# Optimization experiments

Measured on AMD Instinct MI355X. Metric: run time of the kernel, lower is better.

## Reference

```python
import jax, jax.numpy as jnp
import numpy as np

N_NODES = 100000
N_EDGES = 1000000
D = 64            # in_channels == heads*hidden_channels
OUT = 64          # out_channels
L = 3             # local_layers
RVQ = 3           # residual VQ levels per layer
CODES = 16
BN_EPS = 1e-5
COMMIT_W = 0.25


def _l2n(v, eps=1e-12):
    return v / (jnp.linalg.norm(v, axis=-1, keepdims=True) + eps)


def setup_inputs() -> dict:
    key = jax.random.key(0)
    ks = jax.random.split(key, 16)
    s = 1.0 / np.sqrt(D)
    inp = {
        "x": jax.random.normal(ks[0], (N_NODES, D), jnp.float32),
        "edge_index": jax.random.randint(ks[1], (2, N_EDGES), 0, N_NODES, jnp.int64),
        # SAGEConv: lin_l (applied to mean-aggregated neighbors, with bias), lin_r (root, no bias)
        "Wa": jax.random.uniform(ks[2], (L, D, D), jnp.float32, -s, s),
        "ba": jax.random.uniform(ks[3], (L, D), jnp.float32, -s, s),
        "Wr": jax.random.uniform(ks[4], (L, D, D), jnp.float32, -s, s),
        # skip Linear per layer
        "Wl": jax.random.uniform(ks[5], (L, D, D), jnp.float32, -s, s),
        "bl": jax.random.uniform(ks[6], (L, D), jnp.float32, -s, s),
        # BatchNorm affine
        "gamma": jnp.ones((L, D), jnp.float32),
        "beta": jnp.zeros((L, D), jnp.float32),
        # residual-VQ codebooks: [layer, rvq_level, codes, dim]
        "codebooks": jax.random.normal(ks[7], (L, RVQ, CODES, D), jnp.float32),
        # heads
        "Wp": jax.random.uniform(ks[8], (D, OUT), jnp.float32, -s, s),
        "bp": jax.random.uniform(ks[9], (OUT,), jnp.float32, -s, s),
        "Wg": jax.random.uniform(ks[10], (D, L * RVQ), jnp.float32, -s, s),
        "bg": jax.random.uniform(ks[11], (L * RVQ,), jnp.float32, -s, s),
    }
    return inp


def _sage_conv(x, src, dst, Wa, ba, Wr):
    # mean aggregation of source features onto destinations
    summed = jax.ops.segment_sum(x[src], dst, num_segments=N_NODES)
    cnt = jax.ops.segment_sum(jnp.ones((src.shape[0],), x.dtype), dst, num_segments=N_NODES)
    mean = summed / jnp.maximum(cnt, 1.0)[:, None]
    out = mean @ Wa + ba + x @ Wr
    return _l2n(out)  # normalize=True


def _residual_vq(x, cbs):
    # cosine-sim residual VQ, 3 levels; returns (quantized_sum, ids [N,RVQ], commit_loss)
    residual = x
    quant = jnp.zeros_like(x)
    loss = jnp.zeros((), x.dtype)
    ids = []
    for r in range(RVQ):
        cb = _l2n(cbs[r])                       # [CODES, D]
        sim = _l2n(residual) @ cb.T             # [N, CODES]
        idx = jnp.argmax(sim, axis=-1)          # [N]
        q = cb[idx]                             # [N, D]
        loss = loss + COMMIT_W * jnp.mean((jax.lax.stop_gradient(q) - residual) ** 2)
        q_st = residual + jax.lax.stop_gradient(q - residual)  # straight-through
        quant = quant + q_st
        residual = residual - jax.lax.stop_gradient(q)
        ids.append(idx)
    return quant, jnp.stack(ids, axis=1), loss


def reference(x, edge_index, Wa, ba, Wr, Wl, bl, gamma, beta, codebooks, Wp, bp, Wg, bg):
    src, dst = edge_index[0], edge_index[1]
    h = x  # in_dropout: identity at inference
    x_local = jnp.zeros((N_NODES, D), x.dtype)
    total_commit = jnp.zeros((), x.dtype)
    id_list = []
    for i in range(L):
        h = _sage_conv(h, src, dst, Wa[i], ba[i], Wr[i]) + (h @ Wl[i] + bl[i])
        # BatchNorm1d (batch statistics)
        mu = jnp.mean(h, axis=0)
        var = jnp.var(h, axis=0)
        h = (h - mu) * jax.lax.rsqrt(var + BN_EPS) * gamma[i] + beta[i]
        h = jax.nn.relu(h)  # dropout: identity at inference
        x_local = x_local + h
        _, ids, closs = _residual_vq(h, codebooks[i])
        total_commit = total_commit + closs
        id_list.append(ids)
    id_concat = jnp.concatenate(id_list, axis=1)  # [N, L*RVQ]
    gnn_id = x_local @ Wg + bg
    pred = x_local @ Wp + bp
    return (pred, total_commit, id_concat, gnn_id)
```

## Files before the change

kernel.cpp:

```cpp
#include <hip/hip_runtime.h>
#include <math.h>

#define NN 100000
#define NE 1000000
#define D 64
#define L 3
#define RVQ 3
#define CODES 16
#define BN_EPS 1e-5f
#define COMMIT_W 0.25f

#define GRID_A 2048

#define OFS_ROWPTR 0
#define OFS_CNT    100016
#define OFS_CURSOR 200032
#define OFS_BSUMS  300048
#define OFS_BOFFS  300176
#define OFS_STATS  300304
#define OFS_CSR    300800
#define OFS_HA     1300800
#define OFS_HB     7700800
#define OFS_XLOC   14100800
#define OFS_PART   20500800

#define OUT_PRED   0
#define OUT_COMMIT (NN * D)
#define OUT_IDS    (NN * D + 1)
#define OUT_GNN    (NN * D + 1 + NN * (L * RVQ))

static __device__ __forceinline__ float waveSum(float v) {
    #pragma unroll
    for (int off = 32; off; off >>= 1) v += __shfl_xor(v, off, 64);
    return v;
}

__global__ void k_count(const int* __restrict__ dst, int* __restrict__ cnt) {
    int e = blockIdx.x * blockDim.x + threadIdx.x;
    if (e < NE) atomicAdd(&cnt[dst[e]], 1);
}

#define SCAN_B 1024
__global__ void k_scan1(const int* __restrict__ cnt, int* __restrict__ rowptr,
                        int* __restrict__ bsums) {
    __shared__ int sm[SCAN_B];
    int t = threadIdx.x;
    int i = blockIdx.x * SCAN_B + t;
    int v = (i < NN) ? cnt[i] : 0;
    sm[t] = v;
    __syncthreads();
    for (int off = 1; off < SCAN_B; off <<= 1) {
        int add = (t >= off) ? sm[t - off] : 0;
        __syncthreads();
        sm[t] += add;
        __syncthreads();
    }
    if (i < NN) rowptr[i + 1] = sm[t];
    if (t == SCAN_B - 1) bsums[blockIdx.x] = sm[t];
}

__global__ void k_scan2(const int* __restrict__ bsums, int* __restrict__ boffs, int nb) {
    __shared__ int sm[SCAN_B];
    int t = threadIdx.x;
    int orig = (t < nb) ? bsums[t] : 0;
    sm[t] = orig;
    __syncthreads();
    for (int off = 1; off < SCAN_B; off <<= 1) {
        int add = (t >= off) ? sm[t - off] : 0;
        __syncthreads();
        sm[t] += add;
        __syncthreads();
    }
    if (t < nb) boffs[t] = sm[t] - orig;
}

__global__ void k_scan3(int* __restrict__ rowptr, const int* __restrict__ boffs) {
    int i = blockIdx.x * SCAN_B + threadIdx.x;
    if (i < NN) rowptr[i + 1] += boffs[blockIdx.x];
    if (i == 0) rowptr[0] = 0;
}

__global__ void k_cursor(const int* __restrict__ rowptr, int* __restrict__ cursor) {
    int i = blockIdx.x * blockDim.x + threadIdx.x;
    if (i < NN) cursor[i] = rowptr[i];
}

__global__ void k_fill(const int* __restrict__ src, const int* __restrict__ dst,
                       int* __restrict__ cursor, int* __restrict__ csr_src) {
    int e = blockIdx.x * blockDim.x + threadIdx.x;
    if (e < NE) {
        int p = atomicAdd(&cursor[dst[e]], 1);
        csr_src[p] = src[e];
    }
}

__global__ void k_sortrows(const int* __restrict__ rowptr, int* __restrict__ csr) {
    int n = blockIdx.x * blockDim.x + threadIdx.x;
    if (n >= NN) return;
    int r0 = rowptr[n], r1 = rowptr[n + 1];
    for (int i = r0 + 1; i < r1; ++i) {
        int v = csr[i];
        int j = i - 1;
        while (j >= r0 && csr[j] > v) { csr[j + 1] = csr[j]; --j; }
        csr[j + 1] = v;
    }
}

__global__ __launch_bounds__(256) void k_gather(
    const float* __restrict__ h, const int* __restrict__ rowptr,
    const int* __restrict__ csr_src, float* __restrict__ mean_out) {
    int t = threadIdx.x;
    int lane = t & 63, wid = t >> 6;
    int n = blockIdx.x * 4 + wid;
    if (n >= NN) return;

    int r0 = rowptr[n], r1 = rowptr[n + 1];
    float s = 0.f;
    for (int base = r0; base < r1; base += 64) {
        int last = r1 - 1;
        int ii = base + lane;
        int idx = csr_src[(ii <= last) ? ii : last];
        int m = r1 - base;
        if (m > 64) m = 64;
        int j = 0;
        for (; j + 8 <= m; j += 8) {
            int i0 = __shfl(idx, j + 0, 64), i1 = __shfl(idx, j + 1, 64);
            int i2 = __shfl(idx, j + 2, 64), i3 = __shfl(idx, j + 3, 64);
            int i4 = __shfl(idx, j + 4, 64), i5 = __shfl(idx, j + 5, 64);
            int i6 = __shfl(idx, j + 6, 64), i7 = __shfl(idx, j + 7, 64);
            float v0 = h[i0 * D + lane], v1 = h[i1 * D + lane];
            float v2 = h[i2 * D + lane], v3 = h[i3 * D + lane];
            float v4 = h[i4 * D + lane], v5 = h[i5 * D + lane];
            float v6 = h[i6 * D + lane], v7 = h[i7 * D + lane];
            s += v0; s += v1; s += v2; s += v3;
            s += v4; s += v5; s += v6; s += v7;
        }
        for (; j + 4 <= m; j += 4) {
            int i0 = __shfl(idx, j + 0, 64), i1 = __shfl(idx, j + 1, 64);
            int i2 = __shfl(idx, j + 2, 64), i3 = __shfl(idx, j + 3, 64);
            float v0 = h[i0 * D + lane], v1 = h[i1 * D + lane];
            float v2 = h[i2 * D + lane], v3 = h[i3 * D + lane];
            s += v0; s += v1; s += v2; s += v3;
        }
        for (; j < m; ++j) {
            int i0 = __shfl(idx, j, 64);
            s += h[i0 * D + lane];
        }
    }
    float deg = (float)(r1 - r0);
    mean_out[n * D + lane] = s / fmaxf(deg, 1.0f);
}

__global__ __launch_bounds__(256) void k_matvec(
    const float* __restrict__ h, float* __restrict__ hp,
    const float* __restrict__ Wa, const float* __restrict__ ba,
    const float* __restrict__ Wr, const float* __restrict__ Wl,
    const float* __restrict__ bl, float* __restrict__ partials) {
    __shared__ float red[2][4][D];
    __shared__ float lbuf[4][2][128];
    int t = threadIdx.x, lane = t & 63, wid = t >> 6;

    float wa[D], wr[D], wl[D];
    #pragma unroll
    for (int k = 0; k < D; ++k) {
        wa[k] = Wa[k * D + lane];
        wr[k] = Wr[k * D + lane];
        wl[k] = Wl[k * D + lane];
    }
    float bav = ba[lane], blv = bl[lane];

    int wg = blockIdx.x * 4 + wid;
    const int wstep = GRID_A * 4;
    float accS = 0.f, accQ = 0.f;

    int seg = lane >> 4;
    int sl  = lane & 15;

    {
        float4 v = {0.f, 0.f, 0.f, 0.f};
        if (seg == 0)      v = *(const float4*)(hp + (size_t)wg * D + 4 * sl);
        else if (seg == 1) v = *(const float4*)(h  + (size_t)wg * D + 4 * sl);
        if (seg < 2) *(float4*)&lbuf[wid][0][seg * 64 + 4 * sl] = v;
    }

    int p = 0;
    for (int n = wg; n < NN; n += wstep) {
        int nn = n + wstep;
        bool havepf = (nn < NN);
        float4 pf = {0.f, 0.f, 0.f, 0.f};
        if (havepf && seg < 2) {
            const float* srcp = (seg == 0) ? hp : h;
            pf = *(const float4*)(srcp + (size_t)nn * D + 4 * sl);
        }

        const float* mb = &lbuf[wid][p][0];
        const float* hb = &lbuf[wid][p][64];
        float a = 0.f, r = 0.f, lv = 0.f;
        #pragma unroll
        for (int j = 0; j < 16; ++j) {
            float4 m4 = *(const float4*)(mb + 4 * j);
            float4 h4 = *(const float4*)(hb + 4 * j);
            a += m4.x * wa[4 * j + 0]; r += h4.x * wr[4 * j + 0]; lv += h4.x * wl[4 * j + 0];
            a += m4.y * wa[4 * j + 1]; r += h4.y * wr[4 * j + 1]; lv += h4.y * wl[4 * j + 1];
            a += m4.z * wa[4 * j + 2]; r += h4.z * wr[4 * j + 2]; lv += h4.z * wl[4 * j + 2];
            a += m4.w * wa[4 * j + 3]; r += h4.w * wr[4 * j + 3]; lv += h4.w * wl[4 * j + 3];
        }
        float sage = a + bav + r;
        float ss = waveSum(sage * sage);
        float inv = 1.0f / (sqrtf(ss) + 1e-12f);
        float hpv = sage * inv + lv + blv;
        hp[(size_t)n * D + lane] = hpv;
        accS += hpv;
        accQ += hpv * hpv;

        if (havepf && seg < 2)
            *(float4*)&lbuf[wid][p ^ 1][seg * 64 + 4 * sl] = pf;
        p ^= 1;
    }

    red[0][wid][lane] = accS;
    red[1][wid][lane] = accQ;
    __syncthreads();
    if (wid == 0) {
        float s0 = (red[0][0][lane] + red[0][1][lane]) + (red[0][2][lane] + red[0][3][lane]);
        float q0 = (red[1][0][lane] + red[1][1][lane]) + (red[1][2][lane] + red[1][3][lane]);
        partials[blockIdx.x * 128 + lane]      = s0;
        partials[blockIdx.x * 128 + 64 + lane] = q0;
    }
}

__global__ __launch_bounds__(256) void k_red_stats(
    const float* __restrict__ part, float* __restrict__ stats) {
    __shared__ float sm[256];
    int c = blockIdx.x;
    int i = threadIdx.x;
    float s = 0.f;
    #pragma unroll
    for (int k = 0; k < 8; ++k)
        s += part[(size_t)(i * 8 + k) * 128 + c];
    sm[i] = s;
    __syncthreads();
    #pragma unroll
    for (int off = 128; off >= 1; off >>= 1) {
        if (i < off) sm[i] += sm[i + off];
        __syncthreads();
    }
    if (i == 0) stats[c] = sm[0];
}

#define CBSTRIDE 65
__global__ __launch_bounds__(256) void k_layer_b(
    float* __restrict__ hp,
    const float* __restrict__ stats,
    const float* __restrict__ gamma, const float* __restrict__ beta,
    const float* __restrict__ cbs,
    float* __restrict__ x_local,
    float* __restrict__ ids_out,
    int layer, float* __restrict__ commit, int first_layer) {
    __shared__ float scb[RVQ * CODES * CBSTRIDE];
    __shared__ float sres[256];
    __shared__ float sred[4];
    int t = threadIdx.x, lane = t & 63, wid = t >> 6;

    for (int row = wid; row < RVQ * CODES; row += 4) {
        float v = cbs[row * D + lane];
        float ss = waveSum(v * v);
        scb[row * CBSTRIDE + lane] = v / (sqrtf(ss) + 1e-12f);
    }
    __syncthreads();

    int jj = lane & 15, qq = lane >> 4;
    float cbr[RVQ][16];
    #pragma unroll
    for (int r = 0; r < RVQ; ++r)
        #pragma unroll
        for (int tt = 0; tt < 16; ++tt)
            cbr[r][tt] = scb[(r * CODES + jj) * CBSTRIDE + qq * 16 + tt];

    float mu = stats[lane] * (1.0f / NN);
    float var = stats[64 + lane] * (1.0f / NN) - mu * mu;
    float scale = rsqrtf(var + BN_EPS) * gamma[lane];
    float shift = beta[lane] - mu * scale;

    float closs = 0.f;
    int wg = blockIdx.x * 4 + wid;
    int wstep = gridDim.x * 4;

    for (int n = wg; n < NN; n += wstep) {
        float hpv = hp[n * D + lane];
        float hn = fmaxf(hpv * scale + shift, 0.f);
        hp[n * D + lane] = hn;
        if (first_layer) x_local[n * D + lane] = hn;
        else x_local[n * D + lane] += hn;

        float res = hn;
        int bis[RVQ];
        #pragma unroll
        for (int r = 0; r < RVQ; ++r) {
            sres[t] = res;
            float rc[16];
            #pragma unroll
            for (int i = 0; i < 4; ++i) {
                float4 v4 = *((const float4*)&sres[wid * 64 + qq * 16 + 4 * i]);
                rc[4 * i + 0] = v4.x; rc[4 * i + 1] = v4.y;
                rc[4 * i + 2] = v4.z; rc[4 * i + 3] = v4.w;
            }
            float p = 0.f;
            #pragma unroll
            for (int tt = 0; tt < 16; ++tt) p += rc[tt] * cbr[r][tt];
            p += __shfl_xor(p, 16, 64);
            p += __shfl_xor(p, 32, 64);
            float bv = p;
            int bi = jj;
            #pragma unroll
            for (int off = 8; off; off >>= 1) {
                float ov = __shfl_xor(bv, off, 64);
                int oi = __shfl_xor(bi, off, 64);
                if (ov > bv || (ov == bv && oi < bi)) { bv = ov; bi = oi; }
            }
            float q = scb[(r * CODES + bi) * CBSTRIDE + lane];
            float d = q - res;
            closs += d * d;
            res -= q;
            bis[r] = bi;
        }
        if (lane == 0) {
            ids_out[n * (L * RVQ) + layer * RVQ + 0] = (float)bis[0];
            ids_out[n * (L * RVQ) + layer * RVQ + 1] = (float)bis[1];
            ids_out[n * (L * RVQ) + layer * RVQ + 2] = (float)bis[2];
        }
    }

    closs = waveSum(closs);
    if (lane == 0) sred[wid] = closs;
    __syncthreads();
    if (t == 0) {
        float tot = (sred[0] + sred[1]) + (sred[2] + sred[3]);
        atomicAdd(commit, tot * (COMMIT_W / (float)(NN * D)));
    }
}

__global__ __launch_bounds__(256, 2) void k_head(
    const float* __restrict__ x_local,
    const float* __restrict__ Wp, const float* __restrict__ bp,
    const float* __restrict__ Wg, const float* __restrict__ bg,
    float* __restrict__ pred, float* __restrict__ gnn) {
    int t = threadIdx.x, lane = t & 63, wid = t >> 6;
    int jsafe = (lane < 9) ? lane : 0;

    float wp[D], wg[D];
    #pragma unroll
    for (int k = 0; k < D; ++k) {
        wp[k] = Wp[k * D + lane];
        wg[k] = Wg[k * 9 + jsafe];
    }
    float bpv = bp[lane], bgv = bg[jsafe];

    int w = blockIdx.x * 4 + wid;
    int wstep = gridDim.x * 4;
    for (int n = w; n < NN; n += wstep) {
        int nu = __builtin_amdgcn_readfirstlane(n);
        const float4* xrow = (const float4*)(x_local + (size_t)nu * D);
        float p = 0.f, g = 0.f;
        #pragma unroll
        for (int j = 0; j < 16; ++j) {
            float4 x4 = xrow[j];
            p += x4.x * wp[4 * j + 0]; g += x4.x * wg[4 * j + 0];
            p += x4.y * wp[4 * j + 1]; g += x4.y * wg[4 * j + 1];
            p += x4.z * wp[4 * j + 2]; g += x4.z * wg[4 * j + 2];
            p += x4.w * wp[4 * j + 3]; g += x4.w * wg[4 * j + 3];
        }
        pred[(size_t)n * D + lane] = p + bpv;
        if (lane < 9) gnn[(size_t)n * 9 + lane] = g + bgv;
    }
}

extern "C" void kernel_launch(void* const* d_in, const int* in_sizes, int n_in,
                              void* d_out, int out_size, void* d_ws, size_t ws_size,
                              hipStream_t stream) {
    const float* x   = (const float*)d_in[0];
    const int* ei    = (const int*)d_in[1];
    const float* Wa  = (const float*)d_in[2];
    const float* ba  = (const float*)d_in[3];
    const float* Wr  = (const float*)d_in[4];
    const float* Wl  = (const float*)d_in[5];
    const float* bl  = (const float*)d_in[6];
    const float* gamma = (const float*)d_in[7];
    const float* beta  = (const float*)d_in[8];
    const float* cbs = (const float*)d_in[9];
    const float* Wp  = (const float*)d_in[10];
    const float* bp  = (const float*)d_in[11];
    const float* Wg  = (const float*)d_in[12];
    const float* bg  = (const float*)d_in[13];

    const int* src = ei;
    const int* dst = ei + NE;

    int*   ws_i  = (int*)d_ws;
    float* ws_f  = (float*)d_ws;
    int* rowptr  = ws_i + OFS_ROWPTR;
    int* cnt     = ws_i + OFS_CNT;
    int* cursor  = ws_i + OFS_CURSOR;
    int* bsums   = ws_i + OFS_BSUMS;
    int* boffs   = ws_i + OFS_BOFFS;
    float* stats = ws_f + OFS_STATS;
    int* csr_src = ws_i + OFS_CSR;
    float* hA    = ws_f + OFS_HA;
    float* hB    = ws_f + OFS_HB;
    float* xloc  = ws_f + OFS_XLOC;
    float* part  = ws_f + OFS_PART;

    float* out    = (float*)d_out;
    float* pred   = out + OUT_PRED;
    float* commit = out + OUT_COMMIT;
    float* ids    = out + OUT_IDS;
    float* gnn    = out + OUT_GNN;

    hipMemsetAsync(cnt, 0, NN * sizeof(int), stream);
    hipMemsetAsync(commit, 0, sizeof(float), stream);

    k_count<<<(NE + 255) / 256, 256, 0, stream>>>(dst, cnt);
    int nscan = (NN + SCAN_B - 1) / SCAN_B;
    k_scan1<<<nscan, SCAN_B, 0, stream>>>(cnt, rowptr, bsums);
    k_scan2<<<1, SCAN_B, 0, stream>>>(bsums, boffs, nscan);
    k_scan3<<<nscan, SCAN_B, 0, stream>>>(rowptr, boffs);
    k_cursor<<<(NN + 1023) / 1024, 1024, 0, stream>>>(rowptr, cursor);
    k_fill<<<(NE + 255) / 256, 256, 0, stream>>>(src, dst, cursor, csr_src);
    k_sortrows<<<(NN + 255) / 256, 256, 0, stream>>>(rowptr, csr_src);

    const float* hin = x;
    float* bufs[2] = {hA, hB};
    for (int i = 0; i < L; ++i) {
        float* hp = bufs[i & 1];
        k_gather<<<(NN + 3) / 4, 256, 0, stream>>>(hin, rowptr, csr_src, hp);
        k_matvec<<<GRID_A, 256, 0, stream>>>(hin, hp,
                                             Wa + i * D * D, ba + i * D,
                                             Wr + i * D * D, Wl + i * D * D, bl + i * D,
                                             part);
        k_red_stats<<<128, 256, 0, stream>>>(part, stats + i * 128);
        k_layer_b<<<GRID_A, 256, 0, stream>>>(hp, stats + i * 128,
                                              gamma + i * D, beta + i * D,
                                              cbs + i * RVQ * CODES * D,
                                              xloc, ids, i, commit, (i == 0) ? 1 : 0);
        hin = hp;
    }

    k_head<<<2048, 256, 0, stream>>>(xloc, Wp, bp, Wg, bg, pred, gnn);
}
```

Measured before the change: 928.0 us.

## Remap BN+RVQ kernel to four lanes per node with DPP reductions

Reworks the batchnorm/ReLU/residual-VQ kernel so that four lanes handle each node, 16 dims apiece, instead of one wavefront per node. Each lane holds its residual slice in registers and reads codebook rows from shared memory as float4. Partial similarities are combined with quad DPP moves, and the best code is picked serially in registers. BN scale and shift are precomputed into shared memory and the grid now covers every node directly. The aim is to cut the cross-lane shuffles and the shared-memory round-trip per residual level. The cost is more LDS codebook reads per lane and higher register pressure. Argmax tie-breaking still favours the lowest index.

```diff
diff --git a/kernel.cpp b/kernel.cpp
--- a/kernel.cpp
+++ b/kernel.cpp
@@ -33,6 +33,13 @@
     #pragma unroll
     for (int off = 32; off; off >>= 1) v += __shfl_xor(v, off, 64);
     return v;
+}
+
+static __device__ __forceinline__ float qxor1(float v) {
+    return __int_as_float(__builtin_amdgcn_mov_dpp(__float_as_int(v), 0xB1, 0xF, 0xF, 1));
+}
+static __device__ __forceinline__ float qxor2(float v) {
+    return __int_as_float(__builtin_amdgcn_mov_dpp(__float_as_int(v), 0x4E, 0xF, 0xF, 1));
 }
 
 __global__ void k_count(const int* __restrict__ dst, int* __restrict__ cnt) {
@@ -248,7 +255,7 @@
     if (i == 0) stats[c] = sm[0];
 }
 
-#define CBSTRIDE 65
+#define CBSTRIDE 68
 __global__ __launch_bounds__(256) void k_layer_b(
     float* __restrict__ hp,
     const float* __restrict__ stats,
@@ -257,8 +264,9 @@
     float* __restrict__ x_local,
     float* __restrict__ ids_out,
     int layer, float* __restrict__ commit, int first_layer) {
-    __shared__ float scb[RVQ * CODES * CBSTRIDE];
-    __shared__ float sres[256];
+    __shared__ alignas(16) float scb[RVQ * CODES * CBSTRIDE];
+    __shared__ alignas(16) float sscale[D];
+    __shared__ alignas(16) float sshift[D];
     __shared__ float sred[4];
     int t = threadIdx.x, lane = t & 63, wid = t >> 6;
 
@@ -267,67 +275,90 @@
         float ss = waveSum(v * v);
         scb[row * CBSTRIDE + lane] = v / (sqrtf(ss) + 1e-12f);
     }
-    __syncthreads();
-
-    int jj = lane & 15, qq = lane >> 4;
-    float cbr[RVQ][16];
-    #pragma unroll
-    for (int r = 0; r < RVQ; ++r)
+    if (t < D) {
+        float mu = stats[t] * (1.0f / NN);
+        float var = stats[64 + t] * (1.0f / NN) - mu * mu;
+        float scale = rsqrtf(var + BN_EPS) * gamma[t];
+        sscale[t] = scale;
+        sshift[t] = beta[t] - mu * scale;
+    }
+    __syncthreads();
+
+    int gid = blockIdx.x * 256 + t;
+    int node = gid >> 2;
+    int part = t & 3;
+    float closs = 0.f;
+
+    if (node < NN) {
+        float res[16];
+        size_t base = (size_t)node * D + part * 16;
+        const float4* hr = (const float4*)(hp + base);
+        float4* hw = (float4*)(hp + base);
+        float4* xw = (float4*)(x_local + base);
+        const float4* scp = (const float4*)(sscale + part * 16);
+        const float4* shp = (const float4*)(sshift + part * 16);
+
         #pragma unroll
-        for (int tt = 0; tt < 16; ++tt)
-            cbr[r][tt] = scb[(r * CODES + jj) * CBSTRIDE + qq * 16 + tt];
-
-    float mu = stats[lane] * (1.0f / NN);
-    float var = stats[64 + lane] * (1.0f / NN) - mu * mu;
-    float scale = rsqrtf(var + BN_EPS) * gamma[lane];
-    float shift = beta[lane] - mu * scale;
-
-    float closs = 0.f;
-    int wg = blockIdx.x * 4 + wid;
-    int wstep = gridDim.x * 4;
-
-    for (int n = wg; n < NN; n += wstep) {
-        float hpv = hp[n * D + lane];
-        float hn = fmaxf(hpv * scale + shift, 0.f);
-        hp[n * D + lane] = hn;
-        if (first_layer) x_local[n * D + lane] = hn;
-        else x_local[n * D + lane] += hn;
-
-        float res = hn;
+        for (int i = 0; i < 4; ++i) {
+            float4 v = hr[i];
+            float4 sc = scp[i], sh = shp[i];
+            float4 hn;
+            hn.x = fmaxf(v.x * sc.x + sh.x, 0.f);
+            hn.y = fmaxf(v.y * sc.y + sh.y, 0.f);
+            hn.z = fmaxf(v.z * sc.z + sh.z, 0.f);
+            hn.w = fmaxf(v.w * sc.w + sh.w, 0.f);
+            hw[i] = hn;
+            if (first_layer) {
+                xw[i] = hn;
+            } else {
+                float4 xl = xw[i];
+                xl.x += hn.x; xl.y += hn.y; xl.z += hn.z; xl.w += hn.w;
+                xw[i] = xl;
+            }
+            res[4 * i + 0] = hn.x; res[4 * i + 1] = hn.y;
+            res[4 * i + 2] = hn.z; res[4 * i + 3] = hn.w;
+        }
+
         int bis[RVQ];
         #pragma unroll
         for (int r = 0; r < RVQ; ++r) {
-            sres[t] = res;
-            float rc[16];
+            float sims[CODES];
+            #pragma unroll
+            for (int j = 0; j < CODES; ++j) {
+                const float* cr = &scb[(r * CODES + j) * CBSTRIDE + part * 16];
+                float4 c0 = *(const float4*)(cr + 0);
+                float4 c1 = *(const float4*)(cr + 4);
+                float4 c2 = *(const float4*)(cr + 8);
+                float4 c3 = *(const float4*)(cr + 12);
+                float a = res[0] * c0.x;
+                a += res[1] * c0.y;  a += res[2] * c0.z;  a += res[3] * c0.w;
+                a += res[4] * c1.x;  a += res[5] * c1.y;  a += res[6] * c1.z;  a += res[7] * c1.w;
+                a += res[8] * c2.x;  a += res[9] * c2.y;  a += res[10] * c2.z; a += res[11] * c2.w;
+                a += res[12] * c3.x; a += res[13] * c3.y; a += res[14] * c3.z; a += res[15] * c3.w;
+                float b = a + qxor1(a);
+                sims[j] = b + qxor2(b);
+            }
+            float bv = sims[0];
+            int bi = 0;
+            #pragma unroll
+            for (int j = 1; j < CODES; ++j)
+                if (sims[j] > bv) { bv = sims[j]; bi = j; }
+
+            const float* qr = &scb[(r * CODES + bi) * CBSTRIDE + part * 16];
             #pragma unroll
             for (int i = 0; i < 4; ++i) {
-                float4 v4 = *((const float4*)&sres[wid * 64 + qq * 16 + 4 * i]);
-                rc[4 * i + 0] = v4.x; rc[4 * i + 1] = v4.y;
-                rc[4 * i + 2] = v4.z; rc[4 * i + 3] = v4.w;
+                float4 q = *(const float4*)(qr + 4 * i);
+                float d0 = q.x - res[4 * i + 0]; closs += d0 * d0; res[4 * i + 0] = -d0;
+                float d1 = q.y - res[4 * i + 1]; closs += d1 * d1; res[4 * i + 1] = -d1;
+                float d2 = q.z - res[4 * i + 2]; closs += d2 * d2; res[4 * i + 2] = -d2;
+                float d3 = q.w - res[4 * i + 3]; closs += d3 * d3; res[4 * i + 3] = -d3;
             }
-            float p = 0.f;
-            #pragma unroll
-            for (int tt = 0; tt < 16; ++tt) p += rc[tt] * cbr[r][tt];
-            p += __shfl_xor(p, 16, 64);
-            p += __shfl_xor(p, 32, 64);
-            float bv = p;
-            int bi = jj;
-            #pragma unroll
-            for (int off = 8; off; off >>= 1) {
-                float ov = __shfl_xor(bv, off, 64);
-                int oi = __shfl_xor(bi, off, 64);
-                if (ov > bv || (ov == bv && oi < bi)) { bv = ov; bi = oi; }
-            }
-            float q = scb[(r * CODES + bi) * CBSTRIDE + lane];
-            float d = q - res;
-            closs += d * d;
-            res -= q;
             bis[r] = bi;
         }
-        if (lane == 0) {
-            ids_out[n * (L * RVQ) + layer * RVQ + 0] = (float)bis[0];
-            ids_out[n * (L * RVQ) + layer * RVQ + 1] = (float)bis[1];
-            ids_out[n * (L * RVQ) + layer * RVQ + 2] = (float)bis[2];
+        if (part == 0) {
+            ids_out[(size_t)node * (L * RVQ) + layer * RVQ + 0] = (float)bis[0];
+            ids_out[(size_t)node * (L * RVQ) + layer * RVQ + 1] = (float)bis[1];
+            ids_out[(size_t)node * (L * RVQ) + layer * RVQ + 2] = (float)bis[2];
         }
     }
 
@@ -430,6 +461,7 @@
 
     const float* hin = x;
     float* bufs[2] = {hA, hB};
+    const int nblk_b = (NN * 4 + 255) / 256;
     for (int i = 0; i < L; ++i) {
         float* hp = bufs[i & 1];
         k_gather<<<(NN + 3) / 4, 256, 0, stream>>>(hin, rowptr, csr_src, hp);
@@ -438,7 +470,7 @@
                                              Wr + i * D * D, Wl + i * D * D, bl + i * D,
                                              part);
         k_red_stats<<<128, 256, 0, stream>>>(part, stats + i * 128);
-        k_layer_b<<<GRID_A, 256, 0, stream>>>(hp, stats + i * 128,
+        k_layer_b<<<nblk_b, 256, 0, stream>>>(hp, stats + i * 128,
                                               gamma + i * D, beta + i * D,
                                               cbs + i * RVQ * CODES * D,
                                               xloc, ids, i, commit, (i == 0) ? 1 : 0);
```

Result: faster. 851.2 us (-8.3%).
